# Kernel optimization log

Measured on AMD Instinct MI355X. Metric: run time of the kernel, lower is better.

The kernel has to match this reference:

```python
import jax, jax.numpy as jnp
import numpy as np

B, S, HID = 1, 4096, 2048
NH, NKV, HD = 16, 4, 128
BLK, LOCAL, GNB, STRIDE = 64, 4, 2, 4
ROT = 64  # head_dim * rope_partial_rotary_factor(0.5), already even
SCALE = HD ** -0.5
NEG = -1e9


def _block_select(nb):
    """Static local+global key-block selection per query block (mirrors _select_key_blocks)."""
    sels = []
    for bi in range(nb):
        local = list(range(max(0, bi - LOCAL + 1), bi + 1))
        gc = list(range(0, bi + 1, STRIDE))
        if len(gc) > GNB:
            gc = gc[-GNB:]
        if 0 not in gc:
            gc = [0] + gc
        idx = sorted(set(local + gc))
        sels.append([i for i in idx if 0 <= i < nb and i <= bi])
    m = max(len(s) for s in sels)
    idx = np.zeros((nb, m), np.int32)
    valid = np.zeros((nb, m), bool)
    for i, s in enumerate(sels):
        idx[i, :len(s)] = s
        valid[i, :len(s)] = True
    return jnp.asarray(idx), jnp.asarray(valid)


def _rot_half(x):
    h = x.shape[-1] // 2
    return jnp.concatenate([-x[..., h:], x[..., :h]], axis=-1)


def setup_inputs() -> dict:
    key = jax.random.key(0)
    ks = jax.random.split(key, 8)
    w = lambda k, shp: (jax.random.normal(k, shp, jnp.float32) * 0.02)
    return {
        "hidden": jax.random.normal(ks[0], (B, S, HID), jnp.float32),
        "cos": jax.random.uniform(ks[1], (B, S, ROT), jnp.float32, -1.0, 1.0),
        "sin": jax.random.uniform(ks[2], (B, S, ROT), jnp.float32, -1.0, 1.0),
        "Wq": w(ks[3], (HID, NH * HD)),
        "Wk": w(ks[4], (HID, NKV * HD)),
        "Wv": w(ks[5], (HID, NKV * HD)),
        "Wo": w(ks[6], (NH * HD, HID)),
        "attn_mask": jnp.ones((B, S), jnp.float32),
    }


def reference(hidden, cos, sin, Wq, Wk, Wv, Wo, attn_mask):
    b_, s_, _ = hidden.shape
    q = (hidden @ Wq).reshape(b_, s_, NH, HD).transpose(0, 2, 1, 3)   # [B,H,S,d]
    k = (hidden @ Wk).reshape(b_, s_, NKV, HD).transpose(0, 2, 1, 3)  # [B,Hkv,S,d]
    v = (hidden @ Wv).reshape(b_, s_, NKV, HD).transpose(0, 2, 1, 3)

    # partial RoPE on first ROT channels
    c = cos[:, None, :, :]
    sn = sin[:, None, :, :]
    q1, q2 = q[..., :ROT], q[..., ROT:]
    k1, k2 = k[..., :ROT], k[..., ROT:]
    q = jnp.concatenate([q1 * c + _rot_half(q1) * sn, q2], axis=-1)
    k = jnp.concatenate([k1 * c + _rot_half(k1) * sn, k2], axis=-1)

    # repeat_kv (GQA expand: each kv head repeated contiguously)
    rep = NH // NKV
    k = jnp.repeat(k, rep, axis=1)
    v = jnp.repeat(v, rep, axis=1)

    nb = s_ // BLK  # S chosen divisible by BLK (pad_len == 0)
    qb = q.reshape(b_, NH, nb, BLK, HD)
    kb = k.reshape(b_, NH, nb, BLK, HD)
    vb = v.reshape(b_, NH, nb, BLK, HD)

    idx, valid = _block_select(nb)  # [nb, M]
    m = idx.shape[1]
    ksel = kb[:, :, idx]  # [B,H,nb,M,BLK,d]
    vsel = vb[:, :, idx]

    scores = jnp.einsum('bhnqd,bhnmkd->bhnqmk',
                        qb.astype(jnp.float32), ksel.astype(jnp.float32)) * SCALE
    # key-validity (padding) mask, additive as in original
    key_valid = attn_mask.reshape(b_, nb, BLK)
    kvm = key_valid[:, idx]  # [B,nb,M,BLK]
    scores = scores + (1.0 - kvm[:, None, :, None, :, :]) * NEG
    # invalid (padded) selected slots
    scores = jnp.where(valid[None, None, :, None, :, None], scores, NEG)
    # intra-block causal mask on the diagonal block
    intra = jnp.triu(jnp.ones((BLK, BLK), bool), 1)                    # [q,k]
    same = idx == jnp.arange(nb)[:, None]                              # [nb,M]
    diag = same[:, None, :, None] & intra[None, :, None, :]            # [nb,q,M,k]
    scores = jnp.where(diag[None, None], NEG, scores)

    probs = jax.nn.softmax(scores.reshape(b_, NH, nb, BLK, m * BLK), axis=-1)
    vflat = vsel.reshape(b_, NH, nb, m * BLK, HD)
    out = jnp.einsum('bhnqe,bhned->bhnqd', probs.astype(v.dtype), vflat)
    out = out.reshape(b_, NH, s_, HD).transpose(0, 2, 1, 3).reshape(b_, s_, NH * HD)
    return out @ Wo
```

## Files before the change

kernel.cpp:

```cpp
#include <hip/hip_runtime.h>
#include <hip/hip_bf16.h>


typedef short short8 __attribute__((ext_vector_type(8)));
typedef float f32x4  __attribute__((ext_vector_type(4)));

#define NEGV   (-1.0e9f)
#define SCALE  (0.08838834764831845f)

__device__ __forceinline__ void gload16(const void* g, void* l) {
  __builtin_amdgcn_global_load_lds(
      (const __attribute__((address_space(1))) unsigned int*)g,
      (__attribute__((address_space(3))) unsigned int*)l, 16, 0, 0);
}

__device__ __forceinline__ float bf2f(short s) {
  union { unsigned u; float f; } c;
  c.u = ((unsigned)(unsigned short)s) << 16;
  return c.f;
}

__device__ __forceinline__ short f2bf_s(float f) {
  __hip_bfloat16 b = __float2bfloat16(f);
  short s;
  __builtin_memcpy(&s, &b, 2);
  return s;
}

__global__ void prep_all(const float* __restrict__ H, const float* __restrict__ Wq,
                         const float* __restrict__ Wk, const float* __restrict__ Wv,
                         const float* __restrict__ Wo, __hip_bfloat16* __restrict__ X,
                         __hip_bfloat16* __restrict__ Wt, __hip_bfloat16* __restrict__ Wot) {
  __shared__ __hip_bfloat16 tile[64][73];
  int b = blockIdx.x;
  if (b < 8192) {
    size_t t = (size_t)b * 256 + threadIdx.x;
    float4 v = *(const float4*)(H + t * 4);
    __hip_bfloat16* o = X + t * 4;
    o[0] = __float2bfloat16(v.x); o[1] = __float2bfloat16(v.y);
    o[2] = __float2bfloat16(v.z); o[3] = __float2bfloat16(v.w);
    return;
  }
  const float* src; __hip_bfloat16* dst; int C; int idx;
  if (b < 9216)      { src = Wq; dst = Wt;                          C = 2048; idx = b - 8192; }
  else if (b < 9472) { src = Wk; dst = Wt + (size_t)2048 * 2048;    C = 512;  idx = b - 9216; }
  else if (b < 9728) { src = Wv; dst = Wt + (size_t)2560 * 2048;    C = 512;  idx = b - 9472; }
  else               { src = Wo; dst = Wot;                         C = 2048; idx = b - 9728; }
  int r0 = (idx & 31) * 64, c0 = (idx >> 5) * 64;
  int c = threadIdx.x & 63, rq = threadIdx.x >> 6;
#pragma unroll
  for (int i = 0; i < 16; ++i) {
    int r = i * 4 + rq;
    tile[r][c] = __float2bfloat16(src[(size_t)(r0 + r) * C + c0 + c]);
  }
  __syncthreads();
#pragma unroll
  for (int i = 0; i < 16; ++i) {
    int cc = i * 4 + rq;
    dst[(size_t)(c0 + cc) * 2048 + r0 + c] = tile[c][cc];
  }
}

__global__ void transpose_v(const __hip_bfloat16* __restrict__ Vb,
                            __hip_bfloat16* __restrict__ Vt) {
  __shared__ __hip_bfloat16 tile[64][73];
  int s0 = blockIdx.x * 64, c0 = blockIdx.y * 64;
  int c = threadIdx.x & 63, rq = threadIdx.x >> 6;
#pragma unroll
  for (int i = 0; i < 16; ++i) {
    int r = i * 4 + rq;
    tile[r][c] = Vb[(size_t)(s0 + r) * 512 + c0 + c];
  }
  __syncthreads();
#pragma unroll
  for (int i = 0; i < 16; ++i) {
    int cc = i * 4 + rq;
    Vt[(size_t)(c0 + cc) * 4096 + s0 + c] = tile[c][cc];
  }
}

__global__ void rope_inplace(const float* __restrict__ cosb, const float* __restrict__ sinb,
                             __hip_bfloat16* __restrict__ Qb, __hip_bfloat16* __restrict__ Kb) {
  int t = blockIdx.x * 256 + threadIdx.x;
  __hip_bfloat16* p;
  int s;
  if (t < 262144) {
    s = t >> 6;
    int rem = t & 63;
    p = Qb + (size_t)s * 2048 + (rem >> 2) * 128 + (rem & 3) * 8;
  } else {
    int tk = t - 262144;
    s = tk >> 4;
    int rem = tk & 15;
    p = Kb + (size_t)s * 512 + (rem >> 2) * 128 + (rem & 3) * 8;
  }
  const int g8 = (t & 3) * 8;
  const float* cp = cosb + (size_t)s * 64 + g8;
  const float* sp = sinb + (size_t)s * 64 + g8;
  short8 a = *(const short8*)p;
  short8 b = *(const short8*)(p + 32);
  float ca[8], sa[8], cb[8], sb[8];
  *(float4*)&ca[0] = *(const float4*)cp;        *(float4*)&ca[4] = *(const float4*)(cp + 4);
  *(float4*)&cb[0] = *(const float4*)(cp + 32); *(float4*)&cb[4] = *(const float4*)(cp + 36);
  *(float4*)&sa[0] = *(const float4*)sp;        *(float4*)&sa[4] = *(const float4*)(sp + 4);
  *(float4*)&sb[0] = *(const float4*)(sp + 32); *(float4*)&sb[4] = *(const float4*)(sp + 36);
  short8 oa, ob;
#pragma unroll
  for (int i = 0; i < 8; ++i) {
    float av = bf2f(a[i]), bv = bf2f(b[i]);
    oa[i] = f2bf_s(av * ca[i] - bv * sa[i]);
    ob[i] = f2bf_s(bv * cb[i] + av * sb[i]);
  }
  *(short8*)p = oa;
  *(short8*)(p + 32) = ob;
}

__global__ __launch_bounds__(512, 2) void gemm_qkv4p(
    const __hip_bfloat16* __restrict__ A, const __hip_bfloat16* __restrict__ Bt,
    __hip_bfloat16* __restrict__ Qb, __hip_bfloat16* __restrict__ Kb,
    __hip_bfloat16* __restrict__ Vb) {
  const int K = 2048;
  const int tid = threadIdx.x;
  const int wave = tid >> 6, lane = tid & 63;
  const int l15 = lane & 15, lg = lane >> 4;
  const int bm = blockIdx.x, bn = blockIdx.y;
  const int wm = wave >> 2, wn = wave & 3;

  __shared__ __hip_bfloat16 lds[65536];

  f32x4 acc[8][4] = {};
  const int srow = lane >> 3;
  const int sslot = lane & 7;
  const int scol = (sslot ^ srow) * 8;
  const size_t abase = (size_t)bm * 256 * K;
  const size_t bbase = (size_t)bn * 256 * K;
  const int r3 = l15 & 7;

#define STAGE_HALF(SRC, SBASE, HALF, KO, LBASE)                                  \
  {                                                                              \
    _Pragma("unroll")                                                            \
    for (int l = 0; l < 2; ++l) {                                                \
      int chunk = l * 8 + wave;                                                  \
      int row = chunk * 8 + srow;                                                \
      gload16(SRC + (SBASE) + (size_t)((HALF) * 128 + row) * K + (KO) + scol,    \
              &lds[(LBASE) + chunk * 512]);                                      \
    }                                                                            \
  }

  short8 bfr[4][2];
  short8 af[2][2][2];

#define READ_AF(P, Q, BA)                                                        \
  {                                                                              \
    _Pragma("unroll")                                                            \
    for (int m2 = 0; m2 < 2; ++m2)                                               \
      _Pragma("unroll")                                                          \
      for (int ks = 0; ks < 2; ++ks) {                                           \
        int row = ((Q) * 2 + m2) * 16 + l15;                                     \
        int slot = (ks * 4 + lg) ^ r3;                                           \
        af[P][m2][ks] = *(const short8*)&lds[(BA) + row * 64 + slot * 8];        \
      }                                                                          \
  }

#define READ_BF(BB)                                                              \
  {                                                                              \
    _Pragma("unroll")                                                            \
    for (int ni = 0; ni < 4; ++ni)                                               \
      _Pragma("unroll")                                                          \
      for (int ks = 0; ks < 2; ++ks) {                                           \
        int row = (wn & 1) * 64 + ni * 16 + l15;                                 \
        int slot = (ks * 4 + lg) ^ r3;                                           \
        bfr[ni][ks] = *(const short8*)&lds[(BB) + row * 64 + slot * 8];          \
      }                                                                          \
  }

#define MFMA_Q(Q, P)                                                             \
  {                                                                              \
    __builtin_amdgcn_s_setprio(1);                                               \
    _Pragma("unroll")                                                            \
    for (int ks = 0; ks < 2; ++ks)                                               \
      _Pragma("unroll")                                                          \
      for (int m2 = 0; m2 < 2; ++m2)                                             \
        _Pragma("unroll")                                                        \
        for (int ni = 0; ni < 4; ++ni)                                           \
          acc[(Q) * 2 + m2][ni] = __builtin_amdgcn_mfma_f32_16x16x32_bf16(       \
              af[P][m2][ks], bfr[ni][ks], acc[(Q) * 2 + m2][ni], 0, 0, 0);       \
    __builtin_amdgcn_s_setprio(0);                                               \
  }

#define LGKM0()                                                                  \
  asm volatile("s_waitcnt lgkmcnt(0)" ::: "memory");                             \
  __builtin_amdgcn_sched_barrier(0);

  STAGE_HALF(Bt, bbase, 0, 0, 16384);
  STAGE_HALF(Bt, bbase, 1, 0, 24576);
  STAGE_HALF(A, abase, 0, 0, 0);
  STAGE_HALF(A, abase, 1, 0, 8192);
  STAGE_HALF(Bt, bbase, 0, 64, 49152);
  STAGE_HALF(Bt, bbase, 1, 64, 57344);
  asm volatile("s_waitcnt vmcnt(4)" ::: "memory");
  __builtin_amdgcn_sched_barrier(0);
  __builtin_amdgcn_s_barrier();
  {
    const int bA0 = wm * 8192;
    const int bB0 = 16384 + (wn >> 1) * 8192;
    READ_BF(bB0);
    READ_AF(0, 0, bA0);
  }
  LGKM0();

  for (int t = 0; t < 32; ++t) {
    const int buf = (t & 1) * 32768;
    const int nbuf = buf ^ 32768;
    const int bA = buf + wm * 8192;
    if (t + 1 < 32) STAGE_HALF(A, abase, 0, (t + 1) * 64, nbuf);
    __builtin_amdgcn_s_barrier();
    MFMA_Q(0, 0);
    READ_AF(1, 1, bA);
    LGKM0();
    if (t + 1 < 32) STAGE_HALF(A, abase, 1, (t + 1) * 64, nbuf + 8192);
    __builtin_amdgcn_s_barrier();
    MFMA_Q(1, 1);
    READ_AF(0, 2, bA);
    LGKM0();
    if (t + 2 < 32) STAGE_HALF(Bt, bbase, 0, (t + 2) * 64, buf + 16384);
    __builtin_amdgcn_s_barrier();
    MFMA_Q(2, 0);
    READ_AF(1, 3, bA);
    LGKM0();
    if (t + 2 < 32) STAGE_HALF(Bt, bbase, 1, (t + 2) * 64, buf + 24576);
    if (t < 30) asm volatile("s_waitcnt vmcnt(4)" ::: "memory");
    else        asm volatile("s_waitcnt vmcnt(0)" ::: "memory");
    __builtin_amdgcn_sched_barrier(0);
    __builtin_amdgcn_s_barrier();
    MFMA_Q(3, 1);
    if (t + 1 < 32) {
      const int nbA = nbuf + wm * 8192;
      const int nbB = nbuf + 16384 + (wn >> 1) * 8192;
      READ_BF(nbB);
      READ_AF(0, 0, nbA);
    }
    LGKM0();
  }
#undef STAGE_HALF
#undef READ_AF
#undef READ_BF
#undef MFMA_Q
#undef LGKM0

  __hip_bfloat16* dst; int ldc, coff;
  if (bn < 8)       { dst = Qb; ldc = 2048; coff = bn * 256; }
  else if (bn < 10) { dst = Kb; ldc = 512;  coff = bn * 256 - 2048; }
  else              { dst = Vb; ldc = 512;  coff = bn * 256 - 2560; }
#pragma unroll
  for (int m8 = 0; m8 < 8; ++m8)
#pragma unroll
    for (int ni = 0; ni < 4; ++ni) {
      int row = bm * 256 + wm * 128 + m8 * 16 + lg * 4;
      int col = coff + wn * 64 + ni * 16 + l15;
#pragma unroll
      for (int r = 0; r < 4; ++r)
        dst[(size_t)(row + r) * ldc + col] = __float2bfloat16(acc[m8][ni][r]);
    }
}

__global__ __launch_bounds__(256) void gemm_bt(
    const __hip_bfloat16* __restrict__ A, const __hip_bfloat16* __restrict__ Bt,
    float* __restrict__ C, int M, int N, int K) {
  const int tid = threadIdx.x;
  const int wave = tid >> 6, lane = tid & 63;
  const int l15 = lane & 15, lg = lane >> 4;
  const int bm = blockIdx.x, bn = blockIdx.y;
  const int wm = wave >> 1, wn = wave & 1;

  __shared__ __hip_bfloat16 As[128 * 64];
  __shared__ __hip_bfloat16 Bs[128 * 64];

  f32x4 acc[4][4] = {};
  const int lrow = lane >> 3;
  const int lslot = lane & 7;
  const int scol = (lslot ^ lrow) * 8;
  const size_t abase = (size_t)bm * 128 * K;
  const size_t bbase = (size_t)bn * 128 * K;
  const int r3 = l15 & 7;

  for (int k0 = 0; k0 < K; k0 += 64) {
#pragma unroll
    for (int i = 0; i < 4; ++i) {
      int seg = i * 4 + wave;
      int row = seg * 8 + lrow;
      gload16(A + abase + (size_t)row * K + k0 + scol, &As[seg * 512]);
      gload16(Bt + bbase + (size_t)row * K + k0 + scol, &Bs[seg * 512]);
    }
    __syncthreads();
#pragma unroll
    for (int ks = 0; ks < 2; ++ks) {
      const int slot = (ks * 4 + lg) ^ r3;
      short8 af[4], bf[4];
#pragma unroll
      for (int mi = 0; mi < 4; ++mi)
        af[mi] = *(const short8*)&As[(wm * 64 + mi * 16 + l15) * 64 + slot * 8];
#pragma unroll
      for (int ni = 0; ni < 4; ++ni)
        bf[ni] = *(const short8*)&Bs[(wn * 64 + ni * 16 + l15) * 64 + slot * 8];
#pragma unroll
      for (int mi = 0; mi < 4; ++mi)
#pragma unroll
        for (int ni = 0; ni < 4; ++ni)
          acc[mi][ni] = __builtin_amdgcn_mfma_f32_16x16x32_bf16(af[mi], bf[ni], acc[mi][ni], 0, 0, 0);
    }
    __syncthreads();
  }
#pragma unroll
  for (int mi = 0; mi < 4; ++mi)
#pragma unroll
    for (int ni = 0; ni < 4; ++ni) {
      int row = bm * 128 + wm * 64 + mi * 16 + lg * 4;
      int col = bn * 128 + wn * 64 + ni * 16 + l15;
#pragma unroll
      for (int r = 0; r < 4; ++r)
        C[(size_t)(row + r) * N + col] = acc[mi][ni][r];
    }
}

__global__ __launch_bounds__(256, 2) void attn_kernel(
    const __hip_bfloat16* __restrict__ Qb,
    const __hip_bfloat16* __restrict__ Kb,
    const __hip_bfloat16* __restrict__ Vt,
    const float* __restrict__ amask,
    __hip_bfloat16* __restrict__ AO)
{
  const int bid = blockIdx.x;
  const int h = bid & 15;
  const int bi = bid >> 4;
  const int kvh = h >> 2;
  const int tid = threadIdx.x;
  const int wave = tid >> 6, lane = tid & 63;
  const int l15 = lane & 15, lg = lane >> 4;

  int sel[6]; int nsel = 0;
  {
    int gtop = bi >> 2;
    for (int j = 0; j <= bi; ++j) {
      bool pick = (j == 0) || (j >= bi - 3) || (((j & 3) == 0) && ((j >> 2) >= gtop - 1));
      if (pick && nsel < 6) sel[nsel++] = j;
    }
  }

  __shared__ __hip_bfloat16 kvs[128 * 72];
  __shared__ __hip_bfloat16 Pb[64 * 72];

  short8 qf[4];
  {
    const __hip_bfloat16* qbase =
        Qb + (size_t)(bi * 64 + wave * 16 + l15) * 2048 + h * 128 + lg * 8;
#pragma unroll
    for (int ks = 0; ks < 4; ++ks) qf[ks] = *(const short8*)(qbase + ks * 32);
  }

  f32x4 sc[6][4] = {};
#pragma unroll
  for (int j = 0; j < 6; ++j) {
    if (j < nsel) {
      int kb = sel[j];
#pragma unroll
      for (int i = 0; i < 4; ++i) {
        int e = (i * 256 + tid) * 8;
        int r = e >> 7, c = e & 127;
        short8 v = *(const short8*)(Kb + (size_t)(kb * 64 + r) * 512 + kvh * 128 + c);
        *(short8*)&kvs[r * 136 + c] = v;
      }
      __syncthreads();
#pragma unroll
      for (int nf = 0; nf < 4; ++nf)
#pragma unroll
        for (int ks = 0; ks < 4; ++ks) {
          short8 bfr = *(const short8*)&kvs[(nf * 16 + l15) * 136 + ks * 32 + lg * 8];
          sc[j][nf] = __builtin_amdgcn_mfma_f32_16x16x32_bf16(qf[ks], bfr, sc[j][nf], 0, 0, 0);
        }
      __syncthreads();
    }
  }

  float rowmax[4] = {-3.0e38f, -3.0e38f, -3.0e38f, -3.0e38f};
#pragma unroll
  for (int j = 0; j < 6; ++j) {
    if (j >= nsel) continue;
    int kb = sel[j];
#pragma unroll
    for (int nf = 0; nf < 4; ++nf) {
      int keyg = kb * 64 + nf * 16 + l15;
      float mterm = (1.0f - amask[keyg]) * NEGV;
      int keyl = nf * 16 + l15;
#pragma unroll
      for (int r = 0; r < 4; ++r) {
        float s = sc[j][nf][r] * SCALE + mterm;
        if (kb == bi) {
          int qrow = wave * 16 + lg * 4 + r;
          if (keyl > qrow) s = NEGV;
        }
        sc[j][nf][r] = s;
        rowmax[r] = fmaxf(rowmax[r], s);
      }
    }
  }
#pragma unroll
  for (int r = 0; r < 4; ++r) {
    float v = rowmax[r];
    v = fmaxf(v, __shfl_xor(v, 1)); v = fmaxf(v, __shfl_xor(v, 2));
    v = fmaxf(v, __shfl_xor(v, 4)); v = fmaxf(v, __shfl_xor(v, 8));
    rowmax[r] = v;
  }
  float rinv[4] = {0.f, 0.f, 0.f, 0.f};
#pragma unroll
  for (int j = 0; j < 6; ++j) {
    if (j >= nsel) continue;
#pragma unroll
    for (int nf = 0; nf < 4; ++nf)
#pragma unroll
      for (int r = 0; r < 4; ++r) {
        float p = __expf(sc[j][nf][r] - rowmax[r]);
        sc[j][nf][r] = p;
        rinv[r] += p;
      }
  }
#pragma unroll
  for (int r = 0; r < 4; ++r) {
    float v = rinv[r];
    v += __shfl_xor(v, 1); v += __shfl_xor(v, 2);
    v += __shfl_xor(v, 4); v += __shfl_xor(v, 8);
    rinv[r] = 1.0f / v;
  }

  f32x4 oacc[8] = {};
#pragma unroll
  for (int j = 0; j < 6; ++j) {
    if (j < nsel) {
      int kb = sel[j];
#pragma unroll
      for (int nf = 0; nf < 4; ++nf)
#pragma unroll
        for (int r = 0; r < 4; ++r) {
          int qrow = wave * 16 + lg * 4 + r;
          Pb[qrow * 72 + nf * 16 + l15] = __float2bfloat16(sc[j][nf][r] * rinv[r]);
        }
#pragma unroll
      for (int i = 0; i < 4; ++i) {
        int e = (i * 256 + tid) * 8;
        int d = e >> 6, c = e & 63;
        short8 v = *(const short8*)(Vt + (size_t)(kvh * 128 + d) * 4096 + kb * 64 + c);
        *(short8*)&kvs[d * 72 + c] = v;
      }
      __syncthreads();
#pragma unroll
      for (int ks = 0; ks < 2; ++ks) {
        short8 pa = *(const short8*)&Pb[(wave * 16 + l15) * 72 + ks * 32 + lg * 8];
#pragma unroll
        for (int df = 0; df < 8; ++df) {
          short8 vb = *(const short8*)&kvs[(df * 16 + l15) * 72 + ks * 32 + lg * 8];
          oacc[df] = __builtin_amdgcn_mfma_f32_16x16x32_bf16(pa, vb, oacc[df], 0, 0, 0);
        }
      }
      __syncthreads();
    }
  }

#pragma unroll
  for (int df = 0; df < 8; ++df)
#pragma unroll
    for (int r = 0; r < 4; ++r) {
      int qrow = bi * 64 + wave * 16 + lg * 4 + r;
      AO[(size_t)qrow * 2048 + h * 128 + df * 16 + l15] = __float2bfloat16(oacc[df][r]);
    }
}

extern "C" void kernel_launch(void* const* d_in, const int* in_sizes, int n_in,
                              void* d_out, int out_size, void* d_ws, size_t ws_size,
                              hipStream_t stream) {
  const float* hidden = (const float*)d_in[0];
  const float* cosb   = (const float*)d_in[1];
  const float* sinb   = (const float*)d_in[2];
  const float* Wq     = (const float*)d_in[3];
  const float* Wk     = (const float*)d_in[4];
  const float* Wv     = (const float*)d_in[5];
  const float* Wo     = (const float*)d_in[6];
  const float* amask  = (const float*)d_in[7];

  char* ws = (char*)d_ws;
  __hip_bfloat16* Xb   = (__hip_bfloat16*)(ws);
  __hip_bfloat16* Wt   = (__hip_bfloat16*)(ws + 16777216);
  __hip_bfloat16* Wot  = (__hip_bfloat16*)(ws + 29360128);
  __hip_bfloat16* Qb   = (__hip_bfloat16*)(ws + 37748736);
  __hip_bfloat16* Kb   = (__hip_bfloat16*)(ws + 54525952);
  __hip_bfloat16* Vb   = (__hip_bfloat16*)(ws + 58720256);
  __hip_bfloat16* Vt   = (__hip_bfloat16*)(ws + 62914560);
  __hip_bfloat16* AO   = Xb;

  prep_all<<<10752, 256, 0, stream>>>(hidden, Wq, Wk, Wv, Wo, Xb, Wt, Wot);

  gemm_qkv4p<<<dim3(16, 12), 512, 0, stream>>>(Xb, Wt, Qb, Kb, Vb);

  rope_inplace<<<1280, 256, 0, stream>>>(cosb, sinb, Qb, Kb);
  transpose_v<<<dim3(64, 8), 256, 0, stream>>>(Vb, Vt);

  attn_kernel<<<1024, 256, 0, stream>>>(Qb, Kb, Vt, amask, AO);

  gemm_bt<<<dim3(32, 16), 256, 0, stream>>>(AO, Wot, (float*)d_out, 4096, 2048, 2048);
}
```

Baseline: 169.1 us.

## Share KV tiles across GQA heads with online softmax and double-buffered async loads

The attention kernel is restructured so each block covers one KV head and one query block, with 8 waves spanning the 4 query heads of the group times 2 row halves. K and V tiles are loaded once per block and reused by all four heads. Loads use double-buffered direct-to-LDS global loads with XOR swizzle. Softmax becomes an online one with lazy rescaling, and the RoPE and V-transpose kernels are merged into one launch. This cuts redundant KV traffic and launch overhead, at the cost of only 256 blocks and more LDS per block, which may hurt occupancy.

```diff
diff --git a/kernel.cpp b/kernel.cpp
--- a/kernel.cpp
+++ b/kernel.cpp
@@ -61,10 +61,48 @@
   }
 }
 
-__global__ void transpose_v(const __hip_bfloat16* __restrict__ Vb,
-                            __hip_bfloat16* __restrict__ Vt) {
+__global__ void postproc(const float* __restrict__ cosb, const float* __restrict__ sinb,
+                         __hip_bfloat16* __restrict__ Qb, __hip_bfloat16* __restrict__ Kb,
+                         const __hip_bfloat16* __restrict__ Vb, __hip_bfloat16* __restrict__ Vt) {
   __shared__ __hip_bfloat16 tile[64][73];
-  int s0 = blockIdx.x * 64, c0 = blockIdx.y * 64;
+  int blk = blockIdx.x;
+  if (blk < 1280) {
+    int t = blk * 256 + threadIdx.x;
+    __hip_bfloat16* p;
+    int s;
+    if (t < 262144) {
+      s = t >> 6;
+      int rem = t & 63;
+      p = Qb + (size_t)s * 2048 + (rem >> 2) * 128 + (rem & 3) * 8;
+    } else {
+      int tk = t - 262144;
+      s = tk >> 4;
+      int rem = tk & 15;
+      p = Kb + (size_t)s * 512 + (rem >> 2) * 128 + (rem & 3) * 8;
+    }
+    const int g8 = (t & 3) * 8;
+    const float* cp = cosb + (size_t)s * 64 + g8;
+    const float* sp = sinb + (size_t)s * 64 + g8;
+    short8 a = *(const short8*)p;
+    short8 b = *(const short8*)(p + 32);
+    float ca[8], sa[8], cb[8], sb[8];
+    *(float4*)&ca[0] = *(const float4*)cp;        *(float4*)&ca[4] = *(const float4*)(cp + 4);
+    *(float4*)&cb[0] = *(const float4*)(cp + 32); *(float4*)&cb[4] = *(const float4*)(cp + 36);
+    *(float4*)&sa[0] = *(const float4*)sp;        *(float4*)&sa[4] = *(const float4*)(sp + 4);
+    *(float4*)&sb[0] = *(const float4*)(sp + 32); *(float4*)&sb[4] = *(const float4*)(sp + 36);
+    short8 oa, ob;
+#pragma unroll
+    for (int i = 0; i < 8; ++i) {
+      float av = bf2f(a[i]), bv = bf2f(b[i]);
+      oa[i] = f2bf_s(av * ca[i] - bv * sa[i]);
+      ob[i] = f2bf_s(bv * cb[i] + av * sb[i]);
+    }
+    *(short8*)p = oa;
+    *(short8*)(p + 32) = ob;
+    return;
+  }
+  int idx = blk - 1280;
+  int s0 = (idx & 63) * 64, c0 = (idx >> 6) * 64;
   int c = threadIdx.x & 63, rq = threadIdx.x >> 6;
 #pragma unroll
   for (int i = 0; i < 16; ++i) {
@@ -77,42 +115,6 @@
     int cc = i * 4 + rq;
     Vt[(size_t)(c0 + cc) * 4096 + s0 + c] = tile[c][cc];
   }
-}
-
-__global__ void rope_inplace(const float* __restrict__ cosb, const float* __restrict__ sinb,
-                             __hip_bfloat16* __restrict__ Qb, __hip_bfloat16* __restrict__ Kb) {
-  int t = blockIdx.x * 256 + threadIdx.x;
-  __hip_bfloat16* p;
-  int s;
-  if (t < 262144) {
-    s = t >> 6;
-    int rem = t & 63;
-    p = Qb + (size_t)s * 2048 + (rem >> 2) * 128 + (rem & 3) * 8;
-  } else {
-    int tk = t - 262144;
-    s = tk >> 4;
-    int rem = tk & 15;
-    p = Kb + (size_t)s * 512 + (rem >> 2) * 128 + (rem & 3) * 8;
-  }
-  const int g8 = (t & 3) * 8;
-  const float* cp = cosb + (size_t)s * 64 + g8;
-  const float* sp = sinb + (size_t)s * 64 + g8;
-  short8 a = *(const short8*)p;
-  short8 b = *(const short8*)(p + 32);
-  float ca[8], sa[8], cb[8], sb[8];
-  *(float4*)&ca[0] = *(const float4*)cp;        *(float4*)&ca[4] = *(const float4*)(cp + 4);
-  *(float4*)&cb[0] = *(const float4*)(cp + 32); *(float4*)&cb[4] = *(const float4*)(cp + 36);
-  *(float4*)&sa[0] = *(const float4*)sp;        *(float4*)&sa[4] = *(const float4*)(sp + 4);
-  *(float4*)&sb[0] = *(const float4*)(sp + 32); *(float4*)&sb[4] = *(const float4*)(sp + 36);
-  short8 oa, ob;
-#pragma unroll
-  for (int i = 0; i < 8; ++i) {
-    float av = bf2f(a[i]), bv = bf2f(b[i]);
-    oa[i] = f2bf_s(av * ca[i] - bv * sa[i]);
-    ob[i] = f2bf_s(bv * cb[i] + av * sb[i]);
-  }
-  *(short8*)p = oa;
-  *(short8*)(p + 32) = ob;
 }
 
 __global__ __launch_bounds__(512, 2) void gemm_qkv4p(
@@ -323,7 +325,7 @@
     }
 }
 
-__global__ __launch_bounds__(256, 2) void attn_kernel(
+__global__ __launch_bounds__(512, 2) void attn_kernel(
     const __hip_bfloat16* __restrict__ Qb,
     const __hip_bfloat16* __restrict__ Kb,
     const __hip_bfloat16* __restrict__ Vt,
@@ -331,12 +333,14 @@
     __hip_bfloat16* __restrict__ AO)
 {
   const int bid = blockIdx.x;
-  const int h = bid & 15;
-  const int bi = bid >> 4;
-  const int kvh = h >> 2;
+  const int kvh = bid & 3;
+  const int bi  = bid >> 2;
   const int tid = threadIdx.x;
   const int wave = tid >> 6, lane = tid & 63;
   const int l15 = lane & 15, lg = lane >> 4;
+  const int h  = kvh * 4 + (wave >> 1);
+  const int rh = wave & 1;
+  const int q0 = bi * 64 + rh * 32;
 
   int sel[6]; int nsel = 0;
   {
@@ -347,131 +351,172 @@
     }
   }
 
-  __shared__ __hip_bfloat16 kvs[128 * 72];
-  __shared__ __hip_bfloat16 Pb[64 * 72];
-
-  short8 qf[4];
-  {
-    const __hip_bfloat16* qbase =
-        Qb + (size_t)(bi * 64 + wave * 16 + l15) * 2048 + h * 128 + lg * 8;
-#pragma unroll
-    for (int ks = 0; ks < 4; ++ks) qf[ks] = *(const short8*)(qbase + ks * 32);
-  }
-
-  f32x4 sc[6][4] = {};
+  __shared__ __hip_bfloat16 kv[2][16384];
+  __shared__ __hip_bfloat16 Pl[8][2304];
+
+  short8 qf[2][4];
+#pragma unroll
+  for (int mi = 0; mi < 2; ++mi)
+#pragma unroll
+    for (int ks = 0; ks < 4; ++ks)
+      qf[mi][ks] = *(const short8*)(Qb + (size_t)(q0 + mi * 16 + l15) * 2048 +
+                                    h * 128 + ks * 32 + lg * 8);
+
+  float m[2][4], l[2][4];
+  f32x4 oacc[2][8] = {};
+#pragma unroll
+  for (int mi = 0; mi < 2; ++mi)
+#pragma unroll
+    for (int r = 0; r < 4; ++r) { m[mi][r] = -3.0e38f; l[mi][r] = 0.f; }
+
+#define STAGE_KV(KB, BUF)                                                          \
+  {                                                                                \
+    _Pragma("unroll")                                                              \
+    for (int i = 0; i < 2; ++i) {                                                  \
+      int chunk = (i * 8 + wave) * 64 + lane;                                      \
+      int row = chunk >> 4, slot = chunk & 15;                                     \
+      gload16(Kb + (size_t)((KB) * 64 + row) * 512 + kvh * 128 +                   \
+                  ((slot ^ (row & 15)) * 8),                                       \
+              &kv[BUF][(i * 8 + wave) * 512]);                                     \
+    }                                                                              \
+    _Pragma("unroll")                                                              \
+    for (int i = 0; i < 2; ++i) {                                                  \
+      int chunk = (i * 8 + wave) * 64 + lane;                                      \
+      int row = chunk >> 3, slot = chunk & 7;                                      \
+      gload16(Vt + (size_t)(kvh * 128 + row) * 4096 + (KB) * 64 +                  \
+                  ((slot ^ (row & 7)) * 8),                                        \
+              &kv[BUF][8192 + (i * 8 + wave) * 512]);                              \
+    }                                                                              \
+  }
+
+  STAGE_KV(sel[0], 0);
+
 #pragma unroll
   for (int j = 0; j < 6; ++j) {
     if (j < nsel) {
-      int kb = sel[j];
-#pragma unroll
-      for (int i = 0; i < 4; ++i) {
-        int e = (i * 256 + tid) * 8;
-        int r = e >> 7, c = e & 127;
-        short8 v = *(const short8*)(Kb + (size_t)(kb * 64 + r) * 512 + kvh * 128 + c);
-        *(short8*)&kvs[r * 136 + c] = v;
+      const int kb = sel[j];
+      if (j + 1 < nsel) {
+        STAGE_KV(sel[j + 1], (j + 1) & 1);
+        asm volatile("s_waitcnt vmcnt(4)" ::: "memory");
+      } else {
+        asm volatile("s_waitcnt vmcnt(0)" ::: "memory");
       }
-      __syncthreads();
+      __builtin_amdgcn_sched_barrier(0);
+      __builtin_amdgcn_s_barrier();
+      const __hip_bfloat16* kbuf = kv[j & 1];
+
+      f32x4 sc[2][4] = {};
 #pragma unroll
       for (int nf = 0; nf < 4; ++nf)
 #pragma unroll
         for (int ks = 0; ks < 4; ++ks) {
-          short8 bfr = *(const short8*)&kvs[(nf * 16 + l15) * 136 + ks * 32 + lg * 8];
-          sc[j][nf] = __builtin_amdgcn_mfma_f32_16x16x32_bf16(qf[ks], bfr, sc[j][nf], 0, 0, 0);
+          short8 b = *(const short8*)&kbuf[(nf * 16 + l15) * 128 +
+                                           (((ks * 4 + lg) ^ l15) * 8)];
+          sc[0][nf] = __builtin_amdgcn_mfma_f32_16x16x32_bf16(qf[0][ks], b, sc[0][nf], 0, 0, 0);
+          sc[1][nf] = __builtin_amdgcn_mfma_f32_16x16x32_bf16(qf[1][ks], b, sc[1][nf], 0, 0, 0);
         }
-      __syncthreads();
-    }
-  }
-
-  float rowmax[4] = {-3.0e38f, -3.0e38f, -3.0e38f, -3.0e38f};
-#pragma unroll
-  for (int j = 0; j < 6; ++j) {
-    if (j >= nsel) continue;
-    int kb = sel[j];
-#pragma unroll
-    for (int nf = 0; nf < 4; ++nf) {
-      int keyg = kb * 64 + nf * 16 + l15;
-      float mterm = (1.0f - amask[keyg]) * NEGV;
-      int keyl = nf * 16 + l15;
+
+      float am[4];
+#pragma unroll
+      for (int nf = 0; nf < 4; ++nf)
+        am[nf] = (1.0f - amask[kb * 64 + nf * 16 + l15]) * NEGV;
+#pragma unroll
+      for (int mi = 0; mi < 2; ++mi)
+#pragma unroll
+        for (int nf = 0; nf < 4; ++nf) {
+          int keyl = nf * 16 + l15;
+#pragma unroll
+          for (int r = 0; r < 4; ++r) {
+            float s = sc[mi][nf][r] * SCALE + am[nf];
+            if (kb == bi) {
+              int qrow = rh * 32 + mi * 16 + lg * 4 + r;
+              if (keyl > qrow) s = NEGV;
+            }
+            sc[mi][nf][r] = s;
+          }
+        }
+
+      float pm[2][4];
+#pragma unroll
+      for (int mi = 0; mi < 2; ++mi)
+#pragma unroll
+        for (int r = 0; r < 4; ++r) {
+          float v = fmaxf(fmaxf(sc[mi][0][r], sc[mi][1][r]),
+                          fmaxf(sc[mi][2][r], sc[mi][3][r]));
+          v = fmaxf(v, __shfl_xor(v, 1)); v = fmaxf(v, __shfl_xor(v, 2));
+          v = fmaxf(v, __shfl_xor(v, 4)); v = fmaxf(v, __shfl_xor(v, 8));
+          pm[mi][r] = v;
+        }
+
+      bool need = false;
+#pragma unroll
+      for (int mi = 0; mi < 2; ++mi)
+#pragma unroll
+        for (int r = 0; r < 4; ++r) need |= (pm[mi][r] - m[mi][r] > 8.0f);
+      if (__any(need)) {
+#pragma unroll
+        for (int mi = 0; mi < 2; ++mi)
+#pragma unroll
+          for (int r = 0; r < 4; ++r) {
+            float mn = fmaxf(m[mi][r], pm[mi][r]);
+            float scl = __expf(m[mi][r] - mn);
+            l[mi][r] *= scl;
+#pragma unroll
+            for (int df = 0; df < 8; ++df) oacc[mi][df][r] *= scl;
+            m[mi][r] = mn;
+          }
+      }
+
+#pragma unroll
+      for (int mi = 0; mi < 2; ++mi)
+#pragma unroll
+        for (int r = 0; r < 4; ++r) {
+          float rs = 0.f;
+#pragma unroll
+          for (int nf = 0; nf < 4; ++nf) {
+            float p = __expf(sc[mi][nf][r] - m[mi][r]);
+            rs += p;
+            Pl[wave][(mi * 16 + lg * 4 + r) * 72 + nf * 16 + l15] = __float2bfloat16(p);
+          }
+          rs += __shfl_xor(rs, 1); rs += __shfl_xor(rs, 2);
+          rs += __shfl_xor(rs, 4); rs += __shfl_xor(rs, 8);
+          l[mi][r] += rs;
+        }
+
+      short8 af2[2][2];
+#pragma unroll
+      for (int mi = 0; mi < 2; ++mi)
+#pragma unroll
+        for (int ks = 0; ks < 2; ++ks)
+          af2[mi][ks] = *(const short8*)&Pl[wave][(mi * 16 + l15) * 72 + ks * 32 + lg * 8];
+#pragma unroll
+      for (int df = 0; df < 8; ++df)
+#pragma unroll
+        for (int ks = 0; ks < 2; ++ks) {
+          short8 vb = *(const short8*)&kbuf[8192 + (df * 16 + l15) * 64 +
+                                            (((ks * 4 + lg) ^ (l15 & 7)) * 8)];
+          oacc[0][df] = __builtin_amdgcn_mfma_f32_16x16x32_bf16(af2[0][ks], vb, oacc[0][df], 0, 0, 0);
+          oacc[1][df] = __builtin_amdgcn_mfma_f32_16x16x32_bf16(af2[1][ks], vb, oacc[1][df], 0, 0, 0);
+        }
+      __builtin_amdgcn_s_barrier();
+    }
+  }
+#undef STAGE_KV
+
+#pragma unroll
+  for (int mi = 0; mi < 2; ++mi) {
+    float inv[4];
+#pragma unroll
+    for (int r = 0; r < 4; ++r) inv[r] = 1.0f / l[mi][r];
+#pragma unroll
+    for (int df = 0; df < 8; ++df)
 #pragma unroll
       for (int r = 0; r < 4; ++r) {
-        float s = sc[j][nf][r] * SCALE + mterm;
-        if (kb == bi) {
-          int qrow = wave * 16 + lg * 4 + r;
-          if (keyl > qrow) s = NEGV;
-        }
-        sc[j][nf][r] = s;
-        rowmax[r] = fmaxf(rowmax[r], s);
+        int qrow = q0 + mi * 16 + lg * 4 + r;
+        AO[(size_t)qrow * 2048 + h * 128 + df * 16 + l15] =
+            __float2bfloat16(oacc[mi][df][r] * inv[r]);
       }
-    }
-  }
-#pragma unroll
-  for (int r = 0; r < 4; ++r) {
-    float v = rowmax[r];
-    v = fmaxf(v, __shfl_xor(v, 1)); v = fmaxf(v, __shfl_xor(v, 2));
-    v = fmaxf(v, __shfl_xor(v, 4)); v = fmaxf(v, __shfl_xor(v, 8));
-    rowmax[r] = v;
-  }
-  float rinv[4] = {0.f, 0.f, 0.f, 0.f};
-#pragma unroll
-  for (int j = 0; j < 6; ++j) {
-    if (j >= nsel) continue;
-#pragma unroll
-    for (int nf = 0; nf < 4; ++nf)
-#pragma unroll
-      for (int r = 0; r < 4; ++r) {
-        float p = __expf(sc[j][nf][r] - rowmax[r]);
-        sc[j][nf][r] = p;
-        rinv[r] += p;
-      }
-  }
-#pragma unroll
-  for (int r = 0; r < 4; ++r) {
-    float v = rinv[r];
-    v += __shfl_xor(v, 1); v += __shfl_xor(v, 2);
-    v += __shfl_xor(v, 4); v += __shfl_xor(v, 8);
-    rinv[r] = 1.0f / v;
-  }
-
-  f32x4 oacc[8] = {};
-#pragma unroll
-  for (int j = 0; j < 6; ++j) {
-    if (j < nsel) {
-      int kb = sel[j];
-#pragma unroll
-      for (int nf = 0; nf < 4; ++nf)
-#pragma unroll
-        for (int r = 0; r < 4; ++r) {
-          int qrow = wave * 16 + lg * 4 + r;
-          Pb[qrow * 72 + nf * 16 + l15] = __float2bfloat16(sc[j][nf][r] * rinv[r]);
-        }
-#pragma unroll
-      for (int i = 0; i < 4; ++i) {
-        int e = (i * 256 + tid) * 8;
-        int d = e >> 6, c = e & 63;
-        short8 v = *(const short8*)(Vt + (size_t)(kvh * 128 + d) * 4096 + kb * 64 + c);
-        *(short8*)&kvs[d * 72 + c] = v;
-      }
-      __syncthreads();
-#pragma unroll
-      for (int ks = 0; ks < 2; ++ks) {
-        short8 pa = *(const short8*)&Pb[(wave * 16 + l15) * 72 + ks * 32 + lg * 8];
-#pragma unroll
-        for (int df = 0; df < 8; ++df) {
-          short8 vb = *(const short8*)&kvs[(df * 16 + l15) * 72 + ks * 32 + lg * 8];
-          oacc[df] = __builtin_amdgcn_mfma_f32_16x16x32_bf16(pa, vb, oacc[df], 0, 0, 0);
-        }
-      }
-      __syncthreads();
-    }
-  }
-
-#pragma unroll
-  for (int df = 0; df < 8; ++df)
-#pragma unroll
-    for (int r = 0; r < 4; ++r) {
-      int qrow = bi * 64 + wave * 16 + lg * 4 + r;
-      AO[(size_t)qrow * 2048 + h * 128 + df * 16 + l15] = __float2bfloat16(oacc[df][r]);
-    }
+  }
 }
 
 extern "C" void kernel_launch(void* const* d_in, const int* in_sizes, int n_in,
@@ -500,10 +545,9 @@
 
   gemm_qkv4p<<<dim3(16, 12), 512, 0, stream>>>(Xb, Wt, Qb, Kb, Vb);
 
-  rope_inplace<<<1280, 256, 0, stream>>>(cosb, sinb, Qb, Kb);
-  transpose_v<<<dim3(64, 8), 256, 0, stream>>>(Vb, Vt);
-
-  attn_kernel<<<1024, 256, 0, stream>>>(Qb, Kb, Vt, amask, AO);
+  postproc<<<1792, 256, 0, stream>>>(cosb, sinb, Qb, Kb, Vb, Vt);
+
+  attn_kernel<<<256, 512, 0, stream>>>(Qb, Kb, Vt, amask, AO);
 
   gemm_bt<<<dim3(32, 16), 256, 0, stream>>>(AO, Wot, (float*)d_out, 4096, 2048, 2048);
 }
```

After: 165.5 us. 1.02x faster.
